# Performance work log

Measured on AMD Instinct MI355X. Metric: run time of the kernel, lower is better.

## Reference

```python
import jax, jax.numpy as jnp
import numpy as np

B, I, H, O, E, K = 1024, 512, 2048, 512, 8, 2


def setup_inputs() -> dict:
    key = jax.random.key(0)
    k = jax.random.split(key, 7)
    s = 0.02
    return {
        "x": jax.random.normal(k[0], (B, I), dtype=jnp.float32),
        "Wg": jax.random.normal(k[1], (I, E), dtype=jnp.float32) * s,
        "bg": jnp.zeros((E,), dtype=jnp.float32),
        "W1": jax.random.normal(k[2], (E, I, H), dtype=jnp.float32) * s,
        "b1": jnp.zeros((E, H), dtype=jnp.float32),
        "W2": jax.random.normal(k[3], (E, H, O), dtype=jnp.float32) * s,
        "b2": jnp.zeros((E, O), dtype=jnp.float32),
    }


def reference(x, Wg, bg, W1, b1, W2, b2):
    # Gating: linear -> softmax -> top-k -> renormalize (inference path,
    # no dynamic expert creation / sleep bookkeeping).
    logits = x @ Wg + bg                      # [B, E]
    probs = jax.nn.softmax(logits, axis=-1)
    top_w, top_i = jax.lax.top_k(probs, K)    # [B, K]
    top_w = top_w / jnp.sum(top_w, axis=-1, keepdims=True)
    # Dense combine weights: zero for unselected experts -> identical math to
    # the per-expert mask-gather / weighted scatter-add in the torch loop.
    combine = jnp.zeros((x.shape[0], W1.shape[0]), dtype=x.dtype)
    combine = combine.at[jnp.arange(x.shape[0])[:, None], top_i].add(top_w)  # [B, E]
    # Expert MLPs (Linear -> ReLU -> Linear), batched over experts.
    h = jax.nn.relu(jnp.einsum("bi,eih->beh", x, W1) + b1[None])  # [B, E, H]
    y = jnp.einsum("beh,eho->beo", h, W2) + b2[None]              # [B, E, O]
    out = jnp.einsum("be,beo->bo", combine, y)                    # [B, O]
    return out
```

## Files before the change

kernel.cpp:

```cpp
#include <hip/hip_runtime.h>
#include <math.h>


#define B_TOK 1024
#define I_DIM 512
#define H_DIM 2048
#define O_DIM 512
#define E_NUM 8

#define WS_COUNTS   0
#define WS_OFFSETS  32
#define WS_TOK_E    64
#define WS_TOK_W    8256
#define WS_SLOT_TOK 16448
#define WS_SLOT_WT  24640
#define WS_TOK_SLOT 32832
#define WS_XB       65536
#define WS_HB       (WS_XB + 1048576)
#define WS_Y4       (WS_HB + 8388608)

typedef __attribute__((ext_vector_type(8))) __bf16 bf16x8;
typedef __attribute__((ext_vector_type(4))) __bf16 bf16x4;
typedef __attribute__((ext_vector_type(4))) float f32x4;

#define MFMA16 __builtin_amdgcn_mfma_f32_16x16x32_bf16

__global__ __launch_bounds__(256) void gating_kernel(
    const float* __restrict__ x, const float* __restrict__ Wg,
    const float* __restrict__ bg, __bf16* __restrict__ xb,
    int* __restrict__ tok_e, float* __restrict__ tok_w)
{
    const int lane = threadIdx.x & 63;
    const int t = blockIdx.x * 4 + (threadIdx.x >> 6);
    const float4* x4 = (const float4*)(x + (size_t)t * I_DIM);
    float4 va = x4[lane], vb = x4[lane + 64];
    bf16x4 oa, ob;
    oa[0] = (__bf16)va.x; oa[1] = (__bf16)va.y;
    oa[2] = (__bf16)va.z; oa[3] = (__bf16)va.w;
    ob[0] = (__bf16)vb.x; ob[1] = (__bf16)vb.y;
    ob[2] = (__bf16)vb.z; ob[3] = (__bf16)vb.w;
    *(bf16x4*)(xb + (size_t)t * I_DIM + lane * 4) = oa;
    *(bf16x4*)(xb + (size_t)t * I_DIM + 256 + lane * 4) = ob;

    float acc[8];
#pragma unroll
    for (int e = 0; e < 8; ++e) acc[e] = 0.f;
    float xv[8] = {va.x, va.y, va.z, va.w, vb.x, vb.y, vb.z, vb.w};
#pragma unroll
    for (int u = 0; u < 8; ++u) {
        int i = (u < 4) ? (lane * 4 + u) : (256 + lane * 4 + u - 4);
        const float4* wr = (const float4*)(Wg + (size_t)i * 8);
        float4 wa = wr[0], wb2 = wr[1];
        acc[0] = fmaf(xv[u], wa.x, acc[0]);
        acc[1] = fmaf(xv[u], wa.y, acc[1]);
        acc[2] = fmaf(xv[u], wa.z, acc[2]);
        acc[3] = fmaf(xv[u], wa.w, acc[3]);
        acc[4] = fmaf(xv[u], wb2.x, acc[4]);
        acc[5] = fmaf(xv[u], wb2.y, acc[5]);
        acc[6] = fmaf(xv[u], wb2.z, acc[6]);
        acc[7] = fmaf(xv[u], wb2.w, acc[7]);
    }
#pragma unroll
    for (int off = 32; off > 0; off >>= 1)
#pragma unroll
        for (int e = 0; e < 8; ++e)
            acc[e] += __shfl_xor(acc[e], off, 64);
    if (lane == 0) {
        float l[8];
#pragma unroll
        for (int e = 0; e < 8; ++e) l[e] = acc[e] + bg[e];
        int e0 = 0;
        for (int e = 1; e < 8; ++e) if (l[e] > l[e0]) e0 = e;
        int e1 = (e0 == 0) ? 1 : 0;
        for (int e = 0; e < 8; ++e) {
            if (e == e0) continue;
            if (l[e] > l[e1]) e1 = e;
        }
        float w0 = 1.f / (1.f + expf(l[e1] - l[e0]));
        tok_e[t * 2]     = e0;
        tok_e[t * 2 + 1] = e1;
        tok_w[t * 2]     = w0;
        tok_w[t * 2 + 1] = 1.f - w0;
    }
}

__global__ __launch_bounds__(1024) void scatter_kernel(
    const int* __restrict__ tok_e, const float* __restrict__ tok_w,
    int* __restrict__ counts, int* __restrict__ offsets,
    int* __restrict__ slot_token, float* __restrict__ slot_wt,
    int* __restrict__ tok_slot)
{
    __shared__ int hist[8], soff[8], scur[8];
    const int tid = threadIdx.x;
    if (tid < 8) { hist[tid] = 0; scur[tid] = 0; }
    __syncthreads();
    const int e0 = tok_e[tid * 2], e1 = tok_e[tid * 2 + 1];
    atomicAdd(&hist[e0], 1);
    atomicAdd(&hist[e1], 1);
    __syncthreads();
    if (tid == 0) {
        int run = 0;
        for (int e = 0; e < 8; ++e) { soff[e] = run; run += hist[e]; }
    }
    __syncthreads();
    if (tid < 8) { counts[tid] = hist[tid]; offsets[tid] = soff[tid]; }
#pragma unroll
    for (int k = 0; k < 2; ++k) {
        int e = tok_e[tid * 2 + k];
        int pos = atomicAdd(&scur[e], 1);
        int slot = soff[e] + pos;
        slot_token[slot] = tid;
        slot_wt[slot] = tok_w[tid * 2 + k];
        tok_slot[tid * 2 + k] = slot;
    }
}

template <bool IS_FC1>
__global__ __launch_bounds__(512) void moe_gemm(
    const __bf16* __restrict__ A, const float* __restrict__ Wf,
    const float* __restrict__ bias,
    const int* __restrict__ counts, const int* __restrict__ offsets,
    const int* __restrict__ slot_token,
    __bf16* __restrict__ hb, float* __restrict__ y4)
{
    constexpr int NW   = IS_FC1 ? H_DIM : O_DIM;
    constexpr int KW   = IS_FC1 ? I_DIM : H_DIM;
    constexpr int ASTR = IS_FC1 ? I_DIM : H_DIM;

    const int e  = blockIdx.z;
    const int kc = IS_FC1 ? 0 : (int)blockIdx.y;
    const int k0 = kc * 512;
    const int n0 = blockIdx.x * 32;
    const int Me = counts[e];
    if (Me == 0) return;
    const int off = offsets[e];
    const float* W = Wf + (size_t)e * KW * NW;

    __shared__ __align__(16) __bf16 Bs[32 * 520];

    const int tid = threadIdx.x;
    {
        const int bn = tid & 31;
        const int kg = tid >> 5;
        const float* wp = W + (size_t)(k0 + kg * 32) * NW + n0 + bn;
#pragma unroll
        for (int j4 = 0; j4 < 8; ++j4) {
            float v0 = wp[(size_t)(j4 * 4 + 0) * NW];
            float v1 = wp[(size_t)(j4 * 4 + 1) * NW];
            float v2 = wp[(size_t)(j4 * 4 + 2) * NW];
            float v3 = wp[(size_t)(j4 * 4 + 3) * NW];
            bf16x4 o;
            o[0] = (__bf16)v0; o[1] = (__bf16)v1;
            o[2] = (__bf16)v2; o[3] = (__bf16)v3;
            *(bf16x4*)&Bs[bn * 520 + kg * 32 + j4 * 4] = o;
        }
    }
    __syncthreads();

    const int lane = tid & 63, w = tid >> 6;
    const int l15 = lane & 15, q = lane >> 4;

    for (int m0 = w * 32; m0 < Me; m0 += 256) {
        int mA = m0 + l15;      if (mA >= Me) mA = Me - 1;
        int mB = m0 + 16 + l15; if (mB >= Me) mB = Me - 1;
        const __bf16 *a0, *a1;
        if (IS_FC1) {
            a0 = A + (size_t)slot_token[off + mA] * ASTR + q * 8;
            a1 = A + (size_t)slot_token[off + mB] * ASTR + q * 8;
        } else {
            a0 = A + (size_t)(off + mA) * ASTR + k0 + q * 8;
            a1 = A + (size_t)(off + mB) * ASTR + k0 + q * 8;
        }

        f32x4 acc[2][2] = {};
#pragma unroll 4
        for (int ks = 0; ks < 16; ++ks) {
            bf16x8 af0 = *(const bf16x8*)(a0 + ks * 32);
            bf16x8 af1 = *(const bf16x8*)(a1 + ks * 32);
            bf16x8 bf0 = *(const bf16x8*)&Bs[l15 * 520 + ks * 32 + q * 8];
            bf16x8 bf1 = *(const bf16x8*)&Bs[(16 + l15) * 520 + ks * 32 + q * 8];
            acc[0][0] = MFMA16(af0, bf0, acc[0][0], 0, 0, 0);
            acc[0][1] = MFMA16(af0, bf1, acc[0][1], 0, 0, 0);
            acc[1][0] = MFMA16(af1, bf0, acc[1][0], 0, 0, 0);
            acc[1][1] = MFMA16(af1, bf1, acc[1][1], 0, 0, 0);
        }

#pragma unroll
        for (int jj = 0; jj < 2; ++jj) {
            const int gn = n0 + jj * 16 + l15;
            if (IS_FC1) {
                const float bv = bias[e * H_DIM + gn];
#pragma unroll
                for (int i = 0; i < 2; ++i)
#pragma unroll
                    for (int r = 0; r < 4; ++r) {
                        int m = m0 + i * 16 + q * 4 + r;
                        if (m < Me) {
                            float v = acc[i][jj][r] + bv;
                            hb[(size_t)(off + m) * H_DIM + gn] =
                                (__bf16)fmaxf(v, 0.f);
                        }
                    }
            } else {
#pragma unroll
                for (int i = 0; i < 2; ++i)
#pragma unroll
                    for (int r = 0; r < 4; ++r) {
                        int m = m0 + i * 16 + q * 4 + r;
                        if (m < Me)
                            y4[((size_t)kc * 2048 + off + m) * O_DIM + gn] =
                                acc[i][jj][r];
                    }
            }
        }
    }
}

__global__ __launch_bounds__(256) void combine_kernel(
    const float* __restrict__ y4, const float* __restrict__ b2,
    const int* __restrict__ tok_slot, const int* __restrict__ tok_e,
    const float* __restrict__ tok_w, float* __restrict__ out)
{
    const int idx = blockIdx.x * 256 + threadIdx.x;
    const int t = idx >> 7;
    const int c = (idx & 127) * 4;
    float4 sum = {0.f, 0.f, 0.f, 0.f};
#pragma unroll
    for (int k = 0; k < 2; ++k) {
        const int s = tok_slot[t * 2 + k];
        const int e = tok_e[t * 2 + k];
        const float wgt = tok_w[t * 2 + k];
        float4 a = *(const float4*)(b2 + (size_t)e * O_DIM + c);
#pragma unroll
        for (int kc = 0; kc < 4; ++kc) {
            float4 v = *(const float4*)(y4 + ((size_t)kc * 2048 + s) * O_DIM + c);
            a.x += v.x; a.y += v.y; a.z += v.z; a.w += v.w;
        }
        sum.x += wgt * a.x; sum.y += wgt * a.y;
        sum.z += wgt * a.z; sum.w += wgt * a.w;
    }
    *(float4*)(out + (size_t)t * O_DIM + c) = sum;
}

extern "C" void kernel_launch(void* const* d_in, const int* in_sizes, int n_in,
                              void* d_out, int out_size, void* d_ws, size_t ws_size,
                              hipStream_t stream)
{
    const float* x  = (const float*)d_in[0];
    const float* Wg = (const float*)d_in[1];
    const float* bg = (const float*)d_in[2];
    const float* W1 = (const float*)d_in[3];
    const float* b1 = (const float*)d_in[4];
    const float* W2 = (const float*)d_in[5];
    const float* b2 = (const float*)d_in[6];
    float* out = (float*)d_out;
    char* ws = (char*)d_ws;

    int*    counts   = (int*)(ws + WS_COUNTS);
    int*    offsets  = (int*)(ws + WS_OFFSETS);
    int*    tok_e    = (int*)(ws + WS_TOK_E);
    float*  tok_w    = (float*)(ws + WS_TOK_W);
    int*    slot_tok = (int*)(ws + WS_SLOT_TOK);
    float*  slot_wt  = (float*)(ws + WS_SLOT_WT);
    int*    tok_slot = (int*)(ws + WS_TOK_SLOT);
    __bf16* xb       = (__bf16*)(ws + WS_XB);
    __bf16* hb       = (__bf16*)(ws + WS_HB);
    float*  y4       = (float*)(ws + WS_Y4);

    gating_kernel<<<B_TOK / 4, 256, 0, stream>>>(x, Wg, bg, xb, tok_e, tok_w);
    scatter_kernel<<<1, B_TOK, 0, stream>>>(tok_e, tok_w, counts, offsets,
                                            slot_tok, slot_wt, tok_slot);
    moe_gemm<true><<<dim3(64, 1, 8), 512, 0, stream>>>(
        xb, W1, b1, counts, offsets, slot_tok, hb, y4);
    moe_gemm<false><<<dim3(16, 4, 8), 512, 0, stream>>>(
        hb, W2, b2, counts, offsets, slot_tok, hb, y4);
    combine_kernel<<<(B_TOK * O_DIM / 4) / 256, 256, 0, stream>>>(
        y4, b2, tok_slot, tok_e, tok_w, out);
}
```

Baseline: 158.6 us.

## Widen MoE GEMM N-tile, vectorize weight staging, overlap second K-chunk load

Each block now covers 64 output columns instead of 32, halving the grid and doubling B-fragment use per A load. Weights are staged with coalesced float4 row loads packed as bf16 pairs, replacing strided scalar column loads. Staging is split into two K-halves so the first half of the MFMA loop runs while the second half is being written to LDS. The cost is fewer blocks, more accumulator registers, and possible LDS bank conflicts from the bf16x2 transposed writes.

```diff
diff --git a/kernel.cpp b/kernel.cpp
--- a/kernel.cpp
+++ b/kernel.cpp
@@ -21,9 +21,11 @@
 
 typedef __attribute__((ext_vector_type(8))) __bf16 bf16x8;
 typedef __attribute__((ext_vector_type(4))) __bf16 bf16x4;
+typedef __attribute__((ext_vector_type(2))) __bf16 bf16x2;
 typedef __attribute__((ext_vector_type(4))) float f32x4;
 
 #define MFMA16 __builtin_amdgcn_mfma_f32_16x16x32_bf16
+#define BSTR 520
 
 __global__ __launch_bounds__(256) void gating_kernel(
     const float* __restrict__ x, const float* __restrict__ Wg,
@@ -124,46 +126,47 @@
     __bf16* __restrict__ hb, float* __restrict__ y4)
 {
     constexpr int NW   = IS_FC1 ? H_DIM : O_DIM;
-    constexpr int KW   = IS_FC1 ? I_DIM : H_DIM;
     constexpr int ASTR = IS_FC1 ? I_DIM : H_DIM;
 
     const int e  = blockIdx.z;
     const int kc = IS_FC1 ? 0 : (int)blockIdx.y;
     const int k0 = kc * 512;
-    const int n0 = blockIdx.x * 32;
+    const int n0 = blockIdx.x * 64;
     const int Me = counts[e];
     if (Me == 0) return;
     const int off = offsets[e];
-    const float* W = Wf + (size_t)e * KW * NW;
-
-    __shared__ __align__(16) __bf16 Bs[32 * 520];
+    const float* W = Wf + (size_t)e * (IS_FC1 ? I_DIM * H_DIM : H_DIM * O_DIM);
+
+    __shared__ __align__(16) __bf16 Bs[64 * BSTR];
 
     const int tid = threadIdx.x;
-    {
-        const int bn = tid & 31;
-        const int kg = tid >> 5;
-        const float* wp = W + (size_t)(k0 + kg * 32) * NW + n0 + bn;
-#pragma unroll
-        for (int j4 = 0; j4 < 8; ++j4) {
-            float v0 = wp[(size_t)(j4 * 4 + 0) * NW];
-            float v1 = wp[(size_t)(j4 * 4 + 1) * NW];
-            float v2 = wp[(size_t)(j4 * 4 + 2) * NW];
-            float v3 = wp[(size_t)(j4 * 4 + 3) * NW];
-            bf16x4 o;
-            o[0] = (__bf16)v0; o[1] = (__bf16)v1;
-            o[2] = (__bf16)v2; o[3] = (__bf16)v3;
-            *(bf16x4*)&Bs[bn * 520 + kg * 32 + j4 * 4] = o;
-        }
-    }
-    __syncthreads();
-
     const int lane = tid & 63, w = tid >> 6;
     const int l15 = lane & 15, q = lane >> 4;
 
-    for (int m0 = w * 32; m0 < Me; m0 += 256) {
+    auto stage_chunk = [&](int ch) {
+        const int kb = k0 + ch * 256;
+#pragma unroll
+        for (int i = 0; i < 4; ++i) {
+            const int u = tid + 512 * i;
+            const int p = u >> 4, c4 = u & 15;
+            const float* wp = W + (size_t)(kb + 2 * p) * NW + n0 + c4 * 4;
+            float4 r0 = *(const float4*)wp;
+            float4 r1 = *(const float4*)(wp + NW);
+            const float* f0 = (const float*)&r0;
+            const float* f1 = (const float*)&r1;
+#pragma unroll
+            for (int j = 0; j < 4; ++j) {
+                bf16x2 pk;
+                pk[0] = (__bf16)f0[j];
+                pk[1] = (__bf16)f1[j];
+                *(bf16x2*)&Bs[(size_t)(c4 * 4 + j) * BSTR + ch * 256 + 2 * p] = pk;
+            }
+        }
+    };
+
+    auto set_aptr = [&](int m0, const __bf16*& a0, const __bf16*& a1) {
         int mA = m0 + l15;      if (mA >= Me) mA = Me - 1;
         int mB = m0 + 16 + l15; if (mB >= Me) mB = Me - 1;
-        const __bf16 *a0, *a1;
         if (IS_FC1) {
             a0 = A + (size_t)slot_token[off + mA] * ASTR + q * 8;
             a1 = A + (size_t)slot_token[off + mB] * ASTR + q * 8;
@@ -171,22 +174,25 @@
             a0 = A + (size_t)(off + mA) * ASTR + k0 + q * 8;
             a1 = A + (size_t)(off + mB) * ASTR + k0 + q * 8;
         }
-
-        f32x4 acc[2][2] = {};
+    };
+    auto compute = [&](const __bf16* a0, const __bf16* a1,
+                       f32x4 (&acc)[2][4], int ks0, int ks1) {
 #pragma unroll 4
-        for (int ks = 0; ks < 16; ++ks) {
+        for (int ks = ks0; ks < ks1; ++ks) {
             bf16x8 af0 = *(const bf16x8*)(a0 + ks * 32);
             bf16x8 af1 = *(const bf16x8*)(a1 + ks * 32);
-            bf16x8 bf0 = *(const bf16x8*)&Bs[l15 * 520 + ks * 32 + q * 8];
-            bf16x8 bf1 = *(const bf16x8*)&Bs[(16 + l15) * 520 + ks * 32 + q * 8];
-            acc[0][0] = MFMA16(af0, bf0, acc[0][0], 0, 0, 0);
-            acc[0][1] = MFMA16(af0, bf1, acc[0][1], 0, 0, 0);
-            acc[1][0] = MFMA16(af1, bf0, acc[1][0], 0, 0, 0);
-            acc[1][1] = MFMA16(af1, bf1, acc[1][1], 0, 0, 0);
-        }
-
-#pragma unroll
-        for (int jj = 0; jj < 2; ++jj) {
+#pragma unroll
+            for (int jj = 0; jj < 4; ++jj) {
+                bf16x8 bf = *(const bf16x8*)
+                    &Bs[(size_t)(jj * 16 + l15) * BSTR + ks * 32 + q * 8];
+                acc[0][jj] = MFMA16(af0, bf, acc[0][jj], 0, 0, 0);
+                acc[1][jj] = MFMA16(af1, bf, acc[1][jj], 0, 0, 0);
+            }
+        }
+    };
+    auto epilogue = [&](int m0, f32x4 (&acc)[2][4]) {
+#pragma unroll
+        for (int jj = 0; jj < 4; ++jj) {
             const int gn = n0 + jj * 16 + l15;
             if (IS_FC1) {
                 const float bv = bias[e * H_DIM + gn];
@@ -213,6 +219,30 @@
                     }
             }
         }
+    };
+
+    stage_chunk(0);
+    __syncthreads();
+    stage_chunk(1);
+
+    const bool act0 = (w * 32 < Me);
+    int m0 = w * 32;
+    f32x4 acc[2][4] = {};
+    const __bf16 *a0 = nullptr, *a1 = nullptr;
+    if (act0) {
+        set_aptr(m0, a0, a1);
+        compute(a0, a1, acc, 0, 8);
+    }
+    __syncthreads();
+    if (act0) {
+        compute(a0, a1, acc, 8, 16);
+        epilogue(m0, acc);
+    }
+    for (m0 = w * 32 + 256; m0 < Me; m0 += 256) {
+        f32x4 acc2[2][4] = {};
+        set_aptr(m0, a0, a1);
+        compute(a0, a1, acc2, 0, 16);
+        epilogue(m0, acc2);
     }
 }
 
@@ -270,9 +300,9 @@
     gating_kernel<<<B_TOK / 4, 256, 0, stream>>>(x, Wg, bg, xb, tok_e, tok_w);
     scatter_kernel<<<1, B_TOK, 0, stream>>>(tok_e, tok_w, counts, offsets,
                                             slot_tok, slot_wt, tok_slot);
-    moe_gemm<true><<<dim3(64, 1, 8), 512, 0, stream>>>(
+    moe_gemm<true><<<dim3(32, 1, 8), 512, 0, stream>>>(
         xb, W1, b1, counts, offsets, slot_tok, hb, y4);
-    moe_gemm<false><<<dim3(16, 4, 8), 512, 0, stream>>>(
+    moe_gemm<false><<<dim3(8, 4, 8), 512, 0, stream>>>(
         hb, W2, b2, counts, offsets, slot_tok, hb, y4);
     combine_kernel<<<(B_TOK * O_DIM / 4) / 256, 256, 0, stream>>>(
         y4, b2, tok_slot, tok_e, tok_w, out);
```

New measurement: 156.3 us. Within noise of the previous version (-1.4%).
